# Kernel tuning notes

Hardware: AMD Instinct MI355X
Metric: run time of the kernel (lower is better)

The kernel has to match this reference:

```python
import jax, jax.numpy as jnp
import numpy as np

N_HEADS = 16
D_MODEL = 2048
DK = D_MODEL // N_HEADS
SEQ = 2048


def setup_inputs() -> dict:
    key = jax.random.key(0)
    ks = jax.random.split(key, 11)
    s = 0.02
    return {
        "query": jax.random.normal(ks[0], (SEQ, D_MODEL), jnp.float32),
        "key": jax.random.normal(ks[1], (SEQ, D_MODEL), jnp.float32),
        "value": jax.random.normal(ks[2], (SEQ, D_MODEL), jnp.float32),
        # per-head projection weights, stacked over heads: [H, d_model, dk]
        "Wq": jax.random.normal(ks[3], (N_HEADS, D_MODEL, DK), jnp.float32) * s,
        "bq": jnp.zeros((N_HEADS, DK), jnp.float32),
        "Wk": jax.random.normal(ks[4], (N_HEADS, D_MODEL, DK), jnp.float32) * s,
        "bk": jnp.zeros((N_HEADS, DK), jnp.float32),
        "Wv": jax.random.normal(ks[5], (N_HEADS, D_MODEL, DK), jnp.float32) * s,
        "bv": jnp.zeros((N_HEADS, DK), jnp.float32),
        # output projection: [H*dk, d_model]
        "Wo": jax.random.normal(ks[6], (N_HEADS * DK, D_MODEL), jnp.float32) * s,
        "bo": jnp.zeros((D_MODEL,), jnp.float32),
    }


def reference(query, key, value, Wq, bq, Wk, bk, Wv, bv, Wo, bo):
    # Per-head linear projections, batched over heads. q/k/v: [H, S, dk]
    q = jnp.einsum('sd,hdk->hsk', query, Wq) + bq[:, None, :]
    k = jnp.einsum('sd,hdk->hsk', key, Wk) + bk[:, None, :]
    v = jnp.einsum('sd,hdk->hsk', value, Wv) + bv[:, None, :]
    scale = jnp.sqrt(jnp.asarray(DK, q.dtype))
    # scores: [H, S_q, S_k]
    scores = jnp.einsum('hsk,htk->hst', q, k) / scale
    # Faithful to original: Softmax(dim=0) on each 2D [S_q, S_k] matrix
    # -> normalize over the QUERY axis (axis=1 here).
    attn = jax.nn.softmax(scores, axis=1)
    heads = jnp.einsum('hst,htk->hsk', attn, v)  # [H, S, dk]
    # torch.cat(attentions, dim=1): [S, H*dk]
    concat = jnp.transpose(heads, (1, 0, 2)).reshape(SEQ, N_HEADS * DK)
    return concat @ Wo + bo
```

## Files before the change

### kernel.cpp

```cpp
#include <hip/hip_runtime.h>

#define SEQ 2048
#define DMODEL 2048
#define NHEADS 16
#define DKH 128

typedef __bf16 bf16;
typedef __attribute__((ext_vector_type(8))) __bf16 bf16x8;
typedef __attribute__((ext_vector_type(4))) __bf16 bf16x4;
typedef __attribute__((ext_vector_type(4))) float f32x4;

#define AS1 __attribute__((address_space(1)))
#define AS3 __attribute__((address_space(3)))

__device__ __forceinline__ void async_copy16(const void* g, void* l) {
  __builtin_amdgcn_global_load_lds((AS1 void*)(unsigned long long)g,
                                   (AS3 void*)l, 16, 0, 0);
}

__device__ __forceinline__ int swz(int chunk, int row) {
  return (chunk ^ (row & 7)) << 3;
}
__device__ __forceinline__ int swz16(int chunk, int row) {
  return (chunk ^ (row & 15)) << 3;
}

template <typename OutT, bool BIAS>
__global__ __launch_bounds__(256) void gemm_bt(
    const bf16* __restrict__ A, const bf16* __restrict__ B,
    const float* __restrict__ bias, OutT* __restrict__ C,
    int M, int N, int K, int lda, int ldb, int ldo, float scale,
    long long sA, long long sB, long long sC, long long sBias) {
  A += (long long)blockIdx.z * sA;
  B += (long long)blockIdx.z * sB;
  C += (long long)blockIdx.z * sC;
  const float* biasp = BIAS ? (bias + (long long)blockIdx.z * sBias) : nullptr;

  const int m0 = blockIdx.y * 128;
  const int n0 = blockIdx.x * 128;

  __shared__ __align__(16) bf16 As[128 * 64];
  __shared__ __align__(16) bf16 Bs[128 * 64];

  const int tid = threadIdx.x;
  const int wave = tid >> 6;
  const int lane = tid & 63;
  const int srow = wave * 8 + (lane >> 3);
  const int scol = ((lane & 7) ^ (lane >> 3)) * 8;
  const int wr = (wave >> 1) * 64;
  const int wc = (wave & 1) * 64;
  const int lr = lane & 15;
  const int quad = lane >> 4;

  const bf16* ag = A + (long long)(m0 + srow) * lda + scol;
  const bf16* bg = B + (long long)(n0 + srow) * ldb + scol;

  f32x4 acc[4][4];
#pragma unroll
  for (int i = 0; i < 4; ++i)
#pragma unroll
    for (int j = 0; j < 4; ++j) {
      acc[i][j][0] = 0.f; acc[i][j][1] = 0.f;
      acc[i][j][2] = 0.f; acc[i][j][3] = 0.f;
    }

  for (int kt = 0; kt < K; kt += 64) {
#pragma unroll
    for (int i = 0; i < 4; ++i) {
      async_copy16(ag + kt + (long long)i * 32 * lda, As + (i * 32 + wave * 8) * 64);
      async_copy16(bg + kt + (long long)i * 32 * ldb, Bs + (i * 32 + wave * 8) * 64);
    }
    __syncthreads();
#pragma unroll
    for (int kk = 0; kk < 64; kk += 32) {
      bf16x8 af[4], bfr[4];
#pragma unroll
      for (int i = 0; i < 4; ++i) {
        const int ra = wr + i * 16 + lr;
        const int rb = wc + i * 16 + lr;
        af[i]  = *(const bf16x8*)(As + ra * 64 + swz((kk >> 3) + quad, ra));
        bfr[i] = *(const bf16x8*)(Bs + rb * 64 + swz((kk >> 3) + quad, rb));
      }
#pragma unroll
      for (int i = 0; i < 4; ++i)
#pragma unroll
        for (int j = 0; j < 4; ++j)
          acc[i][j] = __builtin_amdgcn_mfma_f32_16x16x32_bf16(af[i], bfr[j], acc[i][j], 0, 0, 0);
    }
    __syncthreads();
  }

#pragma unroll
  for (int j = 0; j < 4; ++j) {
    const int n = n0 + wc + j * 16 + lr;
    const float bv = BIAS ? biasp[n] : 0.f;
#pragma unroll
    for (int i = 0; i < 4; ++i) {
      const int mb = m0 + wr + i * 16 + quad * 4;
#pragma unroll
      for (int r = 0; r < 4; ++r)
        C[(long long)(mb + r) * ldo + n] = (OutT)(acc[i][j][r] * scale + bv);
    }
  }
}

__global__ __launch_bounds__(256) void qk_exp(
    const bf16* __restrict__ q, const bf16* __restrict__ k,
    bf16* __restrict__ E, float* __restrict__ lpart) {
  const int h = blockIdx.z;
  const int m0 = blockIdx.y * 128;
  const int nstrip = blockIdx.x * 512;
  const bf16* A = q + (long long)h * DKH;
  const bf16* B = k + (long long)h * DKH;
  bf16* C = E + (long long)h * SEQ * SEQ;

  __shared__ __align__(16) bf16 As[128 * 128];
  __shared__ __align__(16) bf16 Bs[64 * 128];

  const int tid = threadIdx.x;
  const int wave = tid >> 6;
  const int lane = tid & 63;
  const int wr = (wave >> 1) * 64;
  const int wc = (wave & 1) * 32;
  const int lr = lane & 15;
  const int quad = lane >> 4;
  const float scale = 0.08838834764831845f;

#pragma unroll
  for (int it = 0; it < 8; ++it) {
    const int row = wave * 32 + it * 4 + (lane >> 4);
    const int chunk = (lane & 15) ^ (row & 15);
    async_copy16(A + (long long)(m0 + row) * DMODEL + chunk * 8,
                 As + (wave * 32 + it * 4) * 128);
  }

  for (int nt = 0; nt < 8; ++nt) {
    if (nt) __syncthreads();
#pragma unroll
    for (int it = 0; it < 4; ++it) {
      const int row = wave * 16 + it * 4 + (lane >> 4);
      const int chunk = (lane & 15) ^ (row & 15);
      async_copy16(B + (long long)(nstrip + nt * 64 + row) * DMODEL + chunk * 8,
                   Bs + (wave * 16 + it * 4) * 128);
    }
    __syncthreads();

    f32x4 acc[4][2];
#pragma unroll
    for (int i = 0; i < 4; ++i)
#pragma unroll
      for (int j = 0; j < 2; ++j) {
        acc[i][j][0] = 0.f; acc[i][j][1] = 0.f;
        acc[i][j][2] = 0.f; acc[i][j][3] = 0.f;
      }

#pragma unroll
    for (int kk = 0; kk < 128; kk += 32) {
      bf16x8 af[4], bfr[2];
#pragma unroll
      for (int i = 0; i < 4; ++i) {
        const int ra = wr + i * 16 + lr;
        af[i] = *(const bf16x8*)(As + ra * 128 + swz16((kk >> 3) + quad, ra));
      }
#pragma unroll
      for (int j = 0; j < 2; ++j) {
        const int rb = wc + j * 16 + lr;
        bfr[j] = *(const bf16x8*)(Bs + rb * 128 + swz16((kk >> 3) + quad, rb));
      }
#pragma unroll
      for (int i = 0; i < 4; ++i)
#pragma unroll
        for (int j = 0; j < 2; ++j)
          acc[i][j] = __builtin_amdgcn_mfma_f32_16x16x32_bf16(af[i], bfr[j], acc[i][j], 0, 0, 0);
    }

#pragma unroll
    for (int j = 0; j < 2; ++j) {
      const int n = nstrip + nt * 64 + wc + j * 16 + lr;
      float l_loc = 0.f;
#pragma unroll
      for (int i = 0; i < 4; ++i) {
        const int mb = m0 + wr + i * 16 + quad * 4;
#pragma unroll
        for (int r = 0; r < 4; ++r) {
          bf16 ev = (bf16)__expf(acc[i][j][r] * scale);
          C[(long long)(mb + r) * SEQ + n] = ev;
          l_loc += (float)ev;
        }
      }
      l_loc += __shfl_xor(l_loc, 16, 64);
      l_loc += __shfl_xor(l_loc, 32, 64);
      if (quad == 0)
        lpart[((long long)h * 32 + blockIdx.y * 2 + (wave >> 1)) * SEQ + n] = l_loc;
    }
  }
}

__global__ void sm_sum(const float* __restrict__ lp, float* __restrict__ rvec) {
  const int i = blockIdx.x * 256 + threadIdx.x;
  const int h = i >> 11, t = i & (SEQ - 1);
  float l = 0.f;
#pragma unroll
  for (int rb = 0; rb < 32; ++rb)
    l += lp[((long long)h * 32 + rb) * SEQ + t];
  rvec[i] = 1.f / l;
}

__global__ void vscale(bf16* __restrict__ vt, const float* __restrict__ rvec) {
  const int cg = blockIdx.y;
  const int t0 = threadIdx.x * 8;
  const float* r = rvec + (cg >> 7) * SEQ;
  bf16x8 v = *(const bf16x8*)(vt + (long long)cg * SEQ + t0);
#pragma unroll
  for (int e = 0; e < 8; ++e) v[e] = (bf16)((float)v[e] * r[t0 + e]);
  *(bf16x8*)(vt + (long long)cg * SEQ + t0) = v;
}

__global__ __launch_bounds__(256) void pv_gemm(
    const bf16* __restrict__ Sc, const bf16* __restrict__ VT,
    bf16* __restrict__ O) {
  const int h = blockIdx.y;
  const int m0 = blockIdx.x * 64;
  const bf16* A = Sc + (long long)h * SEQ * SEQ;
  const bf16* B = VT + (long long)h * DKH * SEQ;

  __shared__ __align__(16) bf16 As[64 * 64];
  __shared__ __align__(16) bf16 Bs[128 * 64];

  const int tid = threadIdx.x;
  const int wave = tid >> 6;
  const int lane = tid & 63;
  const int srow = wave * 8 + (lane >> 3);
  const int scol = ((lane & 7) ^ (lane >> 3)) * 8;
  const int wr = (wave >> 1) * 32;
  const int wc = (wave & 1) * 64;
  const int lr = lane & 15;
  const int quad = lane >> 4;

  const bf16* ag = A + (long long)(m0 + srow) * SEQ + scol;
  const bf16* bg = B + (long long)srow * SEQ + scol;

  f32x4 acc[2][4];
#pragma unroll
  for (int i = 0; i < 2; ++i)
#pragma unroll
    for (int j = 0; j < 4; ++j) {
      acc[i][j][0] = 0.f; acc[i][j][1] = 0.f;
      acc[i][j][2] = 0.f; acc[i][j][3] = 0.f;
    }

  for (int kt = 0; kt < SEQ; kt += 64) {
#pragma unroll
    for (int i = 0; i < 2; ++i)
      async_copy16(ag + kt + (long long)i * 32 * SEQ, As + (i * 32 + wave * 8) * 64);
#pragma unroll
    for (int i = 0; i < 4; ++i)
      async_copy16(bg + kt + (long long)i * 32 * SEQ, Bs + (i * 32 + wave * 8) * 64);
    __syncthreads();
#pragma unroll
    for (int kk = 0; kk < 64; kk += 32) {
      bf16x8 af[2], bfr[4];
#pragma unroll
      for (int i = 0; i < 2; ++i) {
        const int ra = wr + i * 16 + lr;
        af[i] = *(const bf16x8*)(As + ra * 64 + swz((kk >> 3) + quad, ra));
      }
#pragma unroll
      for (int j = 0; j < 4; ++j) {
        const int rb = wc + j * 16 + lr;
        bfr[j] = *(const bf16x8*)(Bs + rb * 64 + swz((kk >> 3) + quad, rb));
      }
#pragma unroll
      for (int i = 0; i < 2; ++i)
#pragma unroll
        for (int j = 0; j < 4; ++j)
          acc[i][j] = __builtin_amdgcn_mfma_f32_16x16x32_bf16(af[i], bfr[j], acc[i][j], 0, 0, 0);
    }
    __syncthreads();
  }

#pragma unroll
  for (int j = 0; j < 4; ++j) {
    const int c = h * DKH + wc + j * 16 + lr;
#pragma unroll
    for (int i = 0; i < 2; ++i) {
      const int mb = m0 + wr + i * 16 + quad * 4;
#pragma unroll
      for (int r = 0; r < 4; ++r)
        O[(long long)(mb + r) * DMODEL + c] = (bf16)acc[i][j][r];
    }
  }
}

__global__ void reduce_bias(const float* __restrict__ p, const float* __restrict__ bo,
                            float* __restrict__ out) {
  const long long i = ((long long)blockIdx.x * 256 + threadIdx.x) * 4;
  const float4 a = *(const float4*)(p + i);
  const float4 b = *(const float4*)(p + (long long)SEQ * DMODEL + i);
  const float4 bb = *(const float4*)(bo + (i & (DMODEL - 1)));
  float4 o;
  o.x = a.x + b.x + bb.x; o.y = a.y + b.y + bb.y;
  o.z = a.z + b.z + bb.z; o.w = a.w + b.w + bb.w;
  *(float4*)(out + i) = o;
}

__global__ __launch_bounds__(256) void prep(
    const float* __restrict__ q, const float* __restrict__ k,
    const float* __restrict__ v,
    const float* __restrict__ Wq, const float* __restrict__ Wk,
    const float* __restrict__ Wv, const float* __restrict__ Wo,
    const float* __restrict__ bq, const float* __restrict__ bk,
    const float* __restrict__ bv,
    bf16* __restrict__ Qb, bf16* __restrict__ Wt, bf16* __restrict__ Wot,
    float* __restrict__ biasQKV) {
  __shared__ float tile[32][33];
  const long long elems = (long long)SEQ * DMODEL;
  const int id = blockIdx.x;
  const int tid = threadIdx.x;

  if (id < 12288) {
    const float* src = (id < 4096) ? q : (id < 8192) ? k : v;
    const int t = id >> 12;
    const long long i = (long long)(id & 4095) * 1024 + tid * 4;
    const float4 vv = *(const float4*)(src + i);
    bf16x4 o;
    o[0] = (bf16)vv.x; o[1] = (bf16)vv.y; o[2] = (bf16)vv.z; o[3] = (bf16)vv.w;
    *(bf16x4*)(Qb + (long long)t * elems + i) = o;
    return;
  }
  const int tx = tid & 31, ty = tid >> 5;
  if (id < 24576) {
    const int rel = id - 12288;
    const int z = rel >> 8;
    const int inner = rel & 255;
    const int bx = inner & 3;
    const int by = inner >> 2;
    const int g = z >> 4, hh = z & 15;
    const float* in = (g == 0 ? Wq : (g == 1 ? Wk : Wv)) + (long long)hh * DMODEL * DKH;
    bf16* o = Wt + (long long)z * DMODEL * DKH;
    const int c0 = bx * 32, r0 = by * 32;
#pragma unroll
    for (int j = 0; j < 32; j += 8)
      tile[ty + j][tx] = in[(long long)(r0 + ty + j) * DKH + c0 + tx];
    __syncthreads();
#pragma unroll
    for (int j = 0; j < 32; j += 8)
      o[(long long)(c0 + ty + j) * DMODEL + r0 + tx] = (bf16)tile[tx][ty + j];
    return;
  }
  if (id < 28672) {
    const int rel = id - 24576;
    const int bx = rel & 63, by = rel >> 6;
    const int c0 = bx * 32, r0 = by * 32;
#pragma unroll
    for (int j = 0; j < 32; j += 8)
      tile[ty + j][tx] = Wo[(long long)(r0 + ty + j) * DMODEL + c0 + tx];
    __syncthreads();
#pragma unroll
    for (int j = 0; j < 32; j += 8)
      Wot[(long long)(c0 + ty + j) * DMODEL + r0 + tx] = (bf16)tile[tx][ty + j];
    return;
  }
  {
    const int i = (id - 28672) * 256 + tid;
    if (i < NHEADS * DKH) {
      biasQKV[i] = bq[i];
      biasQKV[NHEADS * DKH + i] = bk[i];
      biasQKV[2 * NHEADS * DKH + i] = bv[i];
    }
  }
}

__global__ void transpose_v(const bf16* __restrict__ in, bf16* __restrict__ out) {
  __shared__ float tile[32][33];
  const int c0 = blockIdx.x * 32, r0 = blockIdx.y * 32;
  const int tx = threadIdx.x, ty = threadIdx.y;
#pragma unroll
  for (int j = 0; j < 32; j += 8)
    tile[ty + j][tx] = (float)in[(long long)(r0 + ty + j) * DMODEL + c0 + tx];
  __syncthreads();
#pragma unroll
  for (int j = 0; j < 32; j += 8)
    out[(long long)(c0 + ty + j) * SEQ + r0 + tx] = (bf16)tile[tx][ty + j];
}

extern "C" void kernel_launch(void* const* d_in, const int* in_sizes, int n_in,
                              void* d_out, int out_size, void* d_ws, size_t ws_size,
                              hipStream_t stream) {
  const float* query = (const float*)d_in[0];
  const float* key_  = (const float*)d_in[1];
  const float* value = (const float*)d_in[2];
  const float* Wq = (const float*)d_in[3];
  const float* bq = (const float*)d_in[4];
  const float* Wk = (const float*)d_in[5];
  const float* bk = (const float*)d_in[6];
  const float* Wv = (const float*)d_in[7];
  const float* bv = (const float*)d_in[8];
  const float* Wo = (const float*)d_in[9];
  const float* bo = (const float*)d_in[10];
  float* out = (float*)d_out;

  const long long elems = (long long)SEQ * DMODEL;
  const long long SZB = elems * 2;

  char* ws = (char*)d_ws;
  bf16* Qb = (bf16*)ws;
  bf16* Wt = (bf16*)(ws + 3 * SZB);
  bf16* scores = (bf16*)ws;
  float* Opart = (float*)ws;
  char* p = ws + (long long)NHEADS * SEQ * SEQ * 2;
  float* biasQKV = (float*)p; p += 32 * 1024;
  bf16* Wot   = (bf16*)p; p += SZB;
  bf16* qkv   = (bf16*)p; p += 3 * SZB;
  bf16* vt    = (bf16*)p; p += SZB;
  bf16* heads = (bf16*)p; p += SZB;
  float* lpart = (float*)p; p += (long long)NHEADS * 32 * SEQ * 4;
  float* rvec  = (float*)p; p += (long long)NHEADS * SEQ * 4;
  if ((size_t)(p - ws) > ws_size) return;

  prep<<<28680, 256, 0, stream>>>(query, key_, value, Wq, Wk, Wv, Wo,
                                  bq, bk, bv, Qb, Wt, Wot, biasQKV);

  gemm_bt<bf16, true><<<dim3(16, 16, 3), 256, 0, stream>>>(
      Qb, Wt, biasQKV, qkv, SEQ, DMODEL, DMODEL, DMODEL, DMODEL, DMODEL, 1.f,
      elems, elems, elems, (long long)DMODEL);

  transpose_v<<<dim3(DMODEL / 32, SEQ / 32), dim3(32, 8), 0, stream>>>(
      qkv + 2 * elems, vt);

  qk_exp<<<dim3(4, 16, NHEADS), 256, 0, stream>>>(qkv, qkv + elems, scores, lpart);

  sm_sum<<<NHEADS * SEQ / 256, 256, 0, stream>>>(lpart, rvec);

  vscale<<<dim3(1, DMODEL), 256, 0, stream>>>(vt, rvec);

  pv_gemm<<<dim3(SEQ / 64, NHEADS), 256, 0, stream>>>(scores, vt, heads);

  gemm_bt<float, false><<<dim3(16, 16, 2), 256, 0, stream>>>(
      heads, Wot, nullptr, Opart, SEQ, DMODEL, 1024, DMODEL, DMODEL, DMODEL, 1.f,
      1024, 1024, elems, 0);

  reduce_bias<<<elems / 1024, 256, 0, stream>>>(Opart, bo, out);
}
```

Baseline: 344.4 us.

## Use 256x256 eight-wave pipelined GEMM with XCD remap for QKV projection

Replaces the 128-tile QKV projection GEMM with a new kernel that uses 256x256 output tiles, 512 threads, and double-buffered LDS filled by async global-to-LDS copies staged across four compute phases. It remaps workgroup IDs so neighbouring tiles land on the same XCD and raises wave priority around the MFMA bursts. The goal is more data reuse per tile and better overlap of loads with compute. In exchange it runs only 192 workgroups, which risks partial occupancy and makes the pipeline harder to keep correct.

```diff
diff --git a/kernel.cpp b/kernel.cpp
--- a/kernel.cpp
+++ b/kernel.cpp
@@ -102,6 +102,140 @@
         C[(long long)(mb + r) * ldo + n] = (OutT)(acc[i][j][r] * scale + bv);
     }
   }
+}
+
+template <typename OutT, bool BIAS>
+__global__ __launch_bounds__(512, 2) void gemm_bt8(
+    const bf16* __restrict__ A, const bf16* __restrict__ B,
+    const float* __restrict__ bias, OutT* __restrict__ C,
+    int K, int lda, int ldb, int ldo, float scale,
+    long long sA, long long sB, long long sC, long long sBias,
+    int gx, int gy) {
+  const int nwg = gridDim.x;
+  int wg = blockIdx.x;
+  wg = (wg & 7) * (nwg >> 3) + (wg >> 3);
+  const int z = wg / (gx * gy);
+  const int rem = wg - z * gx * gy;
+  const int m0 = (rem / gx) * 256;
+  const int n0 = (rem % gx) * 256;
+
+  A += (long long)z * sA;
+  B += (long long)z * sB;
+  C += (long long)z * sC;
+  const float* biasp = BIAS ? (bias + (long long)z * sBias) : nullptr;
+
+  __shared__ __align__(16) bf16 lds[2][2][2][128 * 64];
+
+  const int tid = threadIdx.x;
+  const int wave = tid >> 6;
+  const int lane = tid & 63;
+  const int grow = wave * 8 + (lane >> 3);
+  const int gcol = ((lane & 7) ^ (lane >> 3)) * 8;
+  const int wm = wave >> 2;
+  const int wn = wave & 3;
+  const int lr = lane & 15;
+  const int quad = lane >> 4;
+
+  const bf16* ag = A + (long long)(m0 + grow) * lda + gcol;
+  const bf16* bg = B + (long long)(n0 + grow) * ldb + gcol;
+
+  auto stA = [&](int buf, int half, int kt) {
+#pragma unroll
+    for (int j = 0; j < 2; ++j)
+      async_copy16(ag + (long long)(half * 128 + j * 64) * lda + kt * 64,
+                   &lds[buf][0][half][(j * 64 + wave * 8) * 64]);
+  };
+  auto stB = [&](int buf, int half, int kt) {
+#pragma unroll
+    for (int j = 0; j < 2; ++j)
+      async_copy16(bg + (long long)(half * 128 + j * 64) * ldb + kt * 64,
+                   &lds[buf][1][half][(j * 64 + wave * 8) * 64]);
+  };
+
+  f32x4 acc[2][2][4][2];
+#pragma unroll
+  for (int a = 0; a < 2; ++a)
+#pragma unroll
+    for (int bq = 0; bq < 2; ++bq)
+#pragma unroll
+      for (int i = 0; i < 4; ++i)
+#pragma unroll
+        for (int j = 0; j < 2; ++j) {
+          acc[a][bq][i][j][0] = 0.f; acc[a][bq][i][j][1] = 0.f;
+          acc[a][bq][i][j][2] = 0.f; acc[a][bq][i][j][3] = 0.f;
+        }
+
+  const int NT = K >> 6;
+
+  stA(0, 0, 0); stB(0, 0, 0); stA(0, 1, 0); stB(0, 1, 0);
+  stA(1, 0, 1); stB(1, 0, 1);
+  asm volatile("s_waitcnt vmcnt(4)" ::: "memory");
+  __builtin_amdgcn_s_barrier();
+  asm volatile("" ::: "memory");
+
+  for (int kt = 0; kt < NT; ++kt) {
+    const int b = kt & 1;
+#pragma unroll
+    for (int ph = 0; ph < 4; ++ph) {
+      const int qm = ph >> 1, qn = ph & 1;
+      const bf16* Ah = lds[b][0][qm];
+      const bf16* Bh = lds[b][1][qn];
+      bf16x8 af[4][2], bfr[2][2];
+#pragma unroll
+      for (int fi = 0; fi < 4; ++fi) {
+        const int r = wm * 64 + fi * 16 + lr;
+#pragma unroll
+        for (int k2 = 0; k2 < 2; ++k2)
+          af[fi][k2] = *(const bf16x8*)(Ah + r * 64 + swz(k2 * 4 + quad, r));
+      }
+#pragma unroll
+      for (int fj = 0; fj < 2; ++fj) {
+        const int r = wn * 32 + fj * 16 + lr;
+#pragma unroll
+        for (int k2 = 0; k2 < 2; ++k2)
+          bfr[fj][k2] = *(const bf16x8*)(Bh + r * 64 + swz(k2 * 4 + quad, r));
+      }
+      if (ph == 0)      { if (kt + 1 < NT) stA(b ^ 1, 1, kt + 1); }
+      else if (ph == 1) { if (kt + 1 < NT) stB(b ^ 1, 1, kt + 1); }
+      else if (ph == 2) { if (kt + 2 < NT) stA(b, 0, kt + 2); }
+      else              { if (kt + 2 < NT) stB(b, 0, kt + 2); }
+      __builtin_amdgcn_s_barrier();
+      asm volatile("s_waitcnt lgkmcnt(0)" ::: "memory");
+      __builtin_amdgcn_s_setprio(1);
+#pragma unroll
+      for (int fi = 0; fi < 4; ++fi)
+#pragma unroll
+        for (int fj = 0; fj < 2; ++fj)
+#pragma unroll
+          for (int k2 = 0; k2 < 2; ++k2)
+            acc[qm][qn][fi][fj] = __builtin_amdgcn_mfma_f32_16x16x32_bf16(
+                af[fi][k2], bfr[fj][k2], acc[qm][qn][fi][fj], 0, 0, 0);
+      __builtin_amdgcn_s_setprio(0);
+      if (ph == 3) {
+        if (kt + 2 < NT) asm volatile("s_waitcnt vmcnt(4)" ::: "memory");
+        else             asm volatile("s_waitcnt vmcnt(0)" ::: "memory");
+      }
+      __builtin_amdgcn_s_barrier();
+      asm volatile("" ::: "memory");
+    }
+  }
+
+#pragma unroll
+  for (int qn = 0; qn < 2; ++qn)
+#pragma unroll
+    for (int fj = 0; fj < 2; ++fj) {
+      const int n = n0 + qn * 128 + wn * 32 + fj * 16 + lr;
+      const float bv = BIAS ? biasp[n] : 0.f;
+#pragma unroll
+      for (int qm = 0; qm < 2; ++qm)
+#pragma unroll
+        for (int fi = 0; fi < 4; ++fi) {
+          const int mb = m0 + qm * 128 + wm * 64 + fi * 16 + quad * 4;
+#pragma unroll
+          for (int r = 0; r < 4; ++r)
+            C[(long long)(mb + r) * ldo + n] = (OutT)(acc[qm][qn][fi][fj][r] * scale + bv);
+        }
+    }
 }
 
 __global__ __launch_bounds__(256) void qk_exp(
@@ -421,9 +555,9 @@
   prep<<<28680, 256, 0, stream>>>(query, key_, value, Wq, Wk, Wv, Wo,
                                   bq, bk, bv, Qb, Wt, Wot, biasQKV);
 
-  gemm_bt<bf16, true><<<dim3(16, 16, 3), 256, 0, stream>>>(
-      Qb, Wt, biasQKV, qkv, SEQ, DMODEL, DMODEL, DMODEL, DMODEL, DMODEL, 1.f,
-      elems, elems, elems, (long long)DMODEL);
+  gemm_bt8<bf16, true><<<dim3(192, 1, 1), 512, 0, stream>>>(
+      Qb, Wt, biasQKV, qkv, DMODEL, DMODEL, DMODEL, DMODEL, 1.f,
+      elems, elems, elems, (long long)DMODEL, 8, 8);
 
   transpose_v<<<dim3(DMODEL / 32, SEQ / 32), dim3(32, 8), 0, stream>>>(
       qkv + 2 * elems, vt);
```

Measured after the change: 353.3 us. 1.03x slower.

## Stage exp scores through LDS for coalesced stores and reuse gemm_bt for PV

Applied to the files above, without the earlier changes.

The QK-exp kernel now uses 64-row query tiles instead of 128, doubling the grid and the number of partial column-sum rows. The exponentiated scores are written into a padded LDS tile and then stored as 16-byte vectors per row, replacing scattered 2-byte global stores. The dedicated PV kernel is removed and the generic gemm_bt template is launched per head with 128x128 tiles instead. This adds a barrier per tile and doubles the work in the partial-sum reduction.

```diff
diff --git a/kernel.cpp b/kernel.cpp
--- a/kernel.cpp
+++ b/kernel.cpp
@@ -104,34 +104,36 @@
   }
 }
 
+#define ESTR 72
 __global__ __launch_bounds__(256) void qk_exp(
     const bf16* __restrict__ q, const bf16* __restrict__ k,
     bf16* __restrict__ E, float* __restrict__ lpart) {
   const int h = blockIdx.z;
-  const int m0 = blockIdx.y * 128;
+  const int m0 = blockIdx.y * 64;
   const int nstrip = blockIdx.x * 512;
   const bf16* A = q + (long long)h * DKH;
   const bf16* B = k + (long long)h * DKH;
   bf16* C = E + (long long)h * SEQ * SEQ;
 
-  __shared__ __align__(16) bf16 As[128 * 128];
+  __shared__ __align__(16) bf16 As[64 * 128];
   __shared__ __align__(16) bf16 Bs[64 * 128];
+  __shared__ __align__(16) bf16 Es[64 * ESTR];
 
   const int tid = threadIdx.x;
   const int wave = tid >> 6;
   const int lane = tid & 63;
-  const int wr = (wave >> 1) * 64;
+  const int wr = (wave >> 1) * 32;
   const int wc = (wave & 1) * 32;
   const int lr = lane & 15;
   const int quad = lane >> 4;
   const float scale = 0.08838834764831845f;
 
 #pragma unroll
-  for (int it = 0; it < 8; ++it) {
-    const int row = wave * 32 + it * 4 + (lane >> 4);
+  for (int it = 0; it < 4; ++it) {
+    const int row = wave * 16 + it * 4 + (lane >> 4);
     const int chunk = (lane & 15) ^ (row & 15);
     async_copy16(A + (long long)(m0 + row) * DMODEL + chunk * 8,
-                 As + (wave * 32 + it * 4) * 128);
+                 As + (wave * 16 + it * 4) * 128);
   }
 
   for (int nt = 0; nt < 8; ++nt) {
@@ -145,9 +147,9 @@
     }
     __syncthreads();
 
-    f32x4 acc[4][2];
-#pragma unroll
-    for (int i = 0; i < 4; ++i)
+    f32x4 acc[2][2];
+#pragma unroll
+    for (int i = 0; i < 2; ++i)
 #pragma unroll
       for (int j = 0; j < 2; ++j) {
         acc[i][j][0] = 0.f; acc[i][j][1] = 0.f;
@@ -156,9 +158,9 @@
 
 #pragma unroll
     for (int kk = 0; kk < 128; kk += 32) {
-      bf16x8 af[4], bfr[2];
-#pragma unroll
-      for (int i = 0; i < 4; ++i) {
+      bf16x8 af[2], bfr[2];
+#pragma unroll
+      for (int i = 0; i < 2; ++i) {
         const int ra = wr + i * 16 + lr;
         af[i] = *(const bf16x8*)(As + ra * 128 + swz16((kk >> 3) + quad, ra));
       }
@@ -168,7 +170,7 @@
         bfr[j] = *(const bf16x8*)(Bs + rb * 128 + swz16((kk >> 3) + quad, rb));
       }
 #pragma unroll
-      for (int i = 0; i < 4; ++i)
+      for (int i = 0; i < 2; ++i)
 #pragma unroll
         for (int j = 0; j < 2; ++j)
           acc[i][j] = __builtin_amdgcn_mfma_f32_16x16x32_bf16(af[i], bfr[j], acc[i][j], 0, 0, 0);
@@ -176,22 +178,34 @@
 
 #pragma unroll
     for (int j = 0; j < 2; ++j) {
-      const int n = nstrip + nt * 64 + wc + j * 16 + lr;
+      const int lcol = wc + j * 16 + lr;
+      const int n = nstrip + nt * 64 + lcol;
       float l_loc = 0.f;
 #pragma unroll
-      for (int i = 0; i < 4; ++i) {
-        const int mb = m0 + wr + i * 16 + quad * 4;
+      for (int i = 0; i < 2; ++i) {
+        const int lrb = wr + i * 16 + quad * 4;
 #pragma unroll
         for (int r = 0; r < 4; ++r) {
           bf16 ev = (bf16)__expf(acc[i][j][r] * scale);
-          C[(long long)(mb + r) * SEQ + n] = ev;
+          Es[(lrb + r) * ESTR + lcol] = ev;
           l_loc += (float)ev;
         }
       }
       l_loc += __shfl_xor(l_loc, 16, 64);
       l_loc += __shfl_xor(l_loc, 32, 64);
       if (quad == 0)
-        lpart[((long long)h * 32 + blockIdx.y * 2 + (wave >> 1)) * SEQ + n] = l_loc;
+        lpart[((long long)h * 64 + blockIdx.y * 2 + (wave >> 1)) * SEQ + n] = l_loc;
+    }
+    __syncthreads();
+
+    {
+      const int row = tid >> 2;
+      const int qc = (tid & 3) * 16;
+      const bf16x8 v0 = *(const bf16x8*)(Es + row * ESTR + qc);
+      const bf16x8 v1 = *(const bf16x8*)(Es + row * ESTR + qc + 8);
+      bf16* dst = C + (long long)(m0 + row) * SEQ + nstrip + nt * 64 + qc;
+      *(bf16x8*)dst = v0;
+      *(bf16x8*)(dst + 8) = v1;
     }
   }
 }
@@ -201,8 +215,8 @@
   const int h = i >> 11, t = i & (SEQ - 1);
   float l = 0.f;
 #pragma unroll
-  for (int rb = 0; rb < 32; ++rb)
-    l += lp[((long long)h * 32 + rb) * SEQ + t];
+  for (int rb = 0; rb < 64; ++rb)
+    l += lp[((long long)h * 64 + rb) * SEQ + t];
   rvec[i] = 1.f / l;
 }
 
@@ -214,82 +228,6 @@
 #pragma unroll
   for (int e = 0; e < 8; ++e) v[e] = (bf16)((float)v[e] * r[t0 + e]);
   *(bf16x8*)(vt + (long long)cg * SEQ + t0) = v;
-}
-
-__global__ __launch_bounds__(256) void pv_gemm(
-    const bf16* __restrict__ Sc, const bf16* __restrict__ VT,
-    bf16* __restrict__ O) {
-  const int h = blockIdx.y;
-  const int m0 = blockIdx.x * 64;
-  const bf16* A = Sc + (long long)h * SEQ * SEQ;
-  const bf16* B = VT + (long long)h * DKH * SEQ;
-
-  __shared__ __align__(16) bf16 As[64 * 64];
-  __shared__ __align__(16) bf16 Bs[128 * 64];
-
-  const int tid = threadIdx.x;
-  const int wave = tid >> 6;
-  const int lane = tid & 63;
-  const int srow = wave * 8 + (lane >> 3);
-  const int scol = ((lane & 7) ^ (lane >> 3)) * 8;
-  const int wr = (wave >> 1) * 32;
-  const int wc = (wave & 1) * 64;
-  const int lr = lane & 15;
-  const int quad = lane >> 4;
-
-  const bf16* ag = A + (long long)(m0 + srow) * SEQ + scol;
-  const bf16* bg = B + (long long)srow * SEQ + scol;
-
-  f32x4 acc[2][4];
-#pragma unroll
-  for (int i = 0; i < 2; ++i)
-#pragma unroll
-    for (int j = 0; j < 4; ++j) {
-      acc[i][j][0] = 0.f; acc[i][j][1] = 0.f;
-      acc[i][j][2] = 0.f; acc[i][j][3] = 0.f;
-    }
-
-  for (int kt = 0; kt < SEQ; kt += 64) {
-#pragma unroll
-    for (int i = 0; i < 2; ++i)
-      async_copy16(ag + kt + (long long)i * 32 * SEQ, As + (i * 32 + wave * 8) * 64);
-#pragma unroll
-    for (int i = 0; i < 4; ++i)
-      async_copy16(bg + kt + (long long)i * 32 * SEQ, Bs + (i * 32 + wave * 8) * 64);
-    __syncthreads();
-#pragma unroll
-    for (int kk = 0; kk < 64; kk += 32) {
-      bf16x8 af[2], bfr[4];
-#pragma unroll
-      for (int i = 0; i < 2; ++i) {
-        const int ra = wr + i * 16 + lr;
-        af[i] = *(const bf16x8*)(As + ra * 64 + swz((kk >> 3) + quad, ra));
-      }
-#pragma unroll
-      for (int j = 0; j < 4; ++j) {
-        const int rb = wc + j * 16 + lr;
-        bfr[j] = *(const bf16x8*)(Bs + rb * 64 + swz((kk >> 3) + quad, rb));
-      }
-#pragma unroll
-      for (int i = 0; i < 2; ++i)
-#pragma unroll
-        for (int j = 0; j < 4; ++j)
-          acc[i][j] = __builtin_amdgcn_mfma_f32_16x16x32_bf16(af[i], bfr[j], acc[i][j], 0, 0, 0);
-    }
-    __syncthreads();
-  }
-
-#pragma unroll
-  for (int j = 0; j < 4; ++j) {
-    const int c = h * DKH + wc + j * 16 + lr;
-#pragma unroll
-    for (int i = 0; i < 2; ++i) {
-      const int mb = m0 + wr + i * 16 + quad * 4;
-#pragma unroll
-      for (int r = 0; r < 4; ++r)
-        O[(long long)(mb + r) * DMODEL + c] = (bf16)acc[i][j][r];
-    }
-  }
 }
 
 __global__ void reduce_bias(const float* __restrict__ p, const float* __restrict__ bo,
@@ -414,7 +352,7 @@
   bf16* qkv   = (bf16*)p; p += 3 * SZB;
   bf16* vt    = (bf16*)p; p += SZB;
   bf16* heads = (bf16*)p; p += SZB;
-  float* lpart = (float*)p; p += (long long)NHEADS * 32 * SEQ * 4;
+  float* lpart = (float*)p; p += (long long)NHEADS * 64 * SEQ * 4;
   float* rvec  = (float*)p; p += (long long)NHEADS * SEQ * 4;
   if ((size_t)(p - ws) > ws_size) return;
 
@@ -428,13 +366,15 @@
   transpose_v<<<dim3(DMODEL / 32, SEQ / 32), dim3(32, 8), 0, stream>>>(
       qkv + 2 * elems, vt);
 
-  qk_exp<<<dim3(4, 16, NHEADS), 256, 0, stream>>>(qkv, qkv + elems, scores, lpart);
+  qk_exp<<<dim3(4, 32, NHEADS), 256, 0, stream>>>(qkv, qkv + elems, scores, lpart);
 
   sm_sum<<<NHEADS * SEQ / 256, 256, 0, stream>>>(lpart, rvec);
 
   vscale<<<dim3(1, DMODEL), 256, 0, stream>>>(vt, rvec);
 
-  pv_gemm<<<dim3(SEQ / 64, NHEADS), 256, 0, stream>>>(scores, vt, heads);
+  gemm_bt<bf16, false><<<dim3(1, 16, NHEADS), 256, 0, stream>>>(
+      scores, vt, nullptr, heads, SEQ, DKH, SEQ, SEQ, SEQ, DMODEL, 1.f,
+      (long long)SEQ * SEQ, (long long)DKH * SEQ, (long long)DKH, 0);
 
   gemm_bt<float, false><<<dim3(16, 16, 2), 256, 0, stream>>>(
       heads, Wot, nullptr, Opart, SEQ, DMODEL, 1024, DMODEL, DMODEL, DMODEL, 1.f,
```

Measured after the change: 378.4 us. +9.9%, slower.
